# Kernel tuning notes

Hardware: AMD Instinct MI355X
Metric: run time of the kernel (lower is better)

## Reference

```python
import jax, jax.numpy as jnp
import numpy as np

N_NODES = 100000
INPUT_DIM = 512
OUTPUT_DIM = 128
N_EDGES = 300000


def setup_inputs() -> dict:
    key = jax.random.key(0)
    k1, k2, k3, k4, k5 = jax.random.split(key, 5)
    x = jax.random.normal(k1, (N_NODES, INPUT_DIM), dtype=jnp.float32)
    train_edges = jax.random.randint(k2, (N_EDGES, 2), 0, N_NODES, dtype=jnp.int64)
    train_false_edges = jax.random.randint(k3, (N_EDGES, 2), 0, N_NODES, dtype=jnp.int64)
    # learned params (xavier / kaiming init approximated with uniform fan-based scales)
    limit_w = float(np.sqrt(6.0 / (INPUT_DIM + OUTPUT_DIM)))
    weight = jax.random.uniform(k4, (INPUT_DIM, OUTPUT_DIM), dtype=jnp.float32,
                                minval=-limit_w, maxval=limit_w)
    limit_w3 = float(np.sqrt(6.0 / OUTPUT_DIM) / np.sqrt(2.0))
    weight_three = jax.random.uniform(k5, (OUTPUT_DIM, 1), dtype=jnp.float32,
                                      minval=-limit_w3, maxval=limit_w3)
    return {"x": x, "train_edges": train_edges, "train_false_edges": train_false_edges,
            "weight": weight, "weight_three": weight_three}


def _decode(z, edges, weight_three):
    # gather endpoints, elementwise multiply, matvec against weight_three
    prod = z[edges[:, 0]] * z[edges[:, 1]]  # [E, output_dim]
    return prod @ weight_three               # [E, 1]


def reference(x, train_edges, train_false_edges, weight, weight_three):
    z = x @ weight  # encode: [N, output_dim]
    z1 = _decode(z, train_edges, weight_three)
    z2 = _decode(z, train_false_edges, weight_three)
    return jax.nn.sigmoid(jnp.concatenate((z1, z2), axis=0))
```

## Files before the change

kernel.cpp:

```cpp
#include <hip/hip_runtime.h>
#include <math.h>

#define IN_DIM 512
#define OUT_DIM 128
#define BM 64
#define BK 64
#define NKT (IN_DIM / BK)

typedef __attribute__((ext_vector_type(8))) __bf16 bf16x8;
typedef __attribute__((ext_vector_type(2))) __bf16 bf16x2;
typedef __attribute__((ext_vector_type(4))) float f32x4;
typedef __attribute__((ext_vector_type(2))) float f32x2;

__device__ inline unsigned short f2bf(float f) {
    unsigned u = __float_as_uint(f);
    u += 0x7FFFu + ((u >> 16) & 1u);
    return (unsigned short)(u >> 16);
}

__device__ inline bf16x8 cvt8(const f32x4& lo, const f32x4& hi) {
    bf16x2 p0 = {(__bf16)lo.x, (__bf16)lo.y};
    bf16x2 p1 = {(__bf16)lo.z, (__bf16)lo.w};
    bf16x2 p2 = {(__bf16)hi.x, (__bf16)hi.y};
    bf16x2 p3 = {(__bf16)hi.z, (__bf16)hi.w};
    uint4 u = {__builtin_bit_cast(unsigned, p0), __builtin_bit_cast(unsigned, p1),
               __builtin_bit_cast(unsigned, p2), __builtin_bit_cast(unsigned, p3)};
    return __builtin_bit_cast(bf16x8, u);
}

__device__ inline void gload_lds16(const void* g, void* l) {
    __builtin_amdgcn_global_load_lds(
        (const __attribute__((address_space(1))) void*)g,
        (__attribute__((address_space(3))) void*)l, 16, 0, 0);
}

__global__ void wt2_kernel(const float* __restrict__ w, unsigned short* __restrict__ wt2) {
    int idx = blockIdx.x * 256 + threadIdx.x;
    int k = idx >> 7;
    int n = idx & 127;
    wt2[(((k >> 3) * 128) + n) * 8 + (k & 7)] = f2bf(w[idx]);
}

__global__ __launch_bounds__(256, 2) void gemm_mfma(const float* __restrict__ x,
                                                    const unsigned short* __restrict__ wt2,
                                                    unsigned short* __restrict__ zb,
                                                    int M) {
    __shared__ float sA[4][BM * BK / 4 * 4];
    char* const pAb = (char*)sA;

    const int tid  = threadIdx.x;
    const int lane = tid & 63;
    const int wid  = tid >> 6;
    const int wm   = wid >> 1;
    const int wn   = wid & 1;
    const int block_row = blockIdx.x * BM;

    const int fr  = lane & 15;
    const int fk4 = lane >> 4;

    f32x4 acc[2][4];
#pragma unroll
    for (int i = 0; i < 2; ++i)
#pragma unroll
        for (int j = 0; j < 4; ++j) acc[i][j] = (f32x4){0.f, 0.f, 0.f, 0.f};

    const int s_row = lane >> 4;
    const int s_cb  = (lane & 15) * 16;

    const int rowa0 = wm * 32 + fr;
    const int rowa1 = rowa0 + 16;
    const int swz7  = (fr & 7) << 5;

    const unsigned short* pb = wt2 + fk4 * 1024 + (wn * 64 + fr) * 8;

#define STAGE(T, B)                                                              \
    {                                                                            \
        _Pragma("unroll") for (int i = 0; i < 4; ++i) {                          \
            const int rr = (wid * 4 + i) * 4 + s_row;                            \
            int grow = block_row + rr;                                           \
            grow = (grow < M) ? grow : (M - 1);                                  \
            const char* src = (const char*)x + (size_t)grow * 2048 +             \
                              (T) * 256 + (s_cb ^ ((rr & 7) << 5));              \
            gload_lds16(src, pAb + (B) * 16384 + (wid * 4 + i) * 1024);          \
        }                                                                        \
    }

#define WAITB(N)                                                                 \
    {                                                                            \
        asm volatile("s_waitcnt vmcnt(" #N ")" ::: "memory");                    \
        __builtin_amdgcn_sched_barrier(0);                                       \
        __builtin_amdgcn_s_barrier();                                            \
        __builtin_amdgcn_sched_barrier(0);                                       \
    }

#define COMP(T, B)                                                               \
    {                                                                            \
        const char* pT = pAb + (B) * 16384;                                      \
        _Pragma("unroll") for (int ks = 0; ks < 2; ++ks) {                       \
            const int cb0 = ks * 128 + fk4 * 32;                                 \
            f32x4 lo0 = *(const f32x4*)(pT + rowa0 * 256 + (cb0 ^ swz7));        \
            f32x4 hi0 = *(const f32x4*)(pT + rowa0 * 256 + (cb0 ^ swz7) + 16);   \
            f32x4 lo1 = *(const f32x4*)(pT + rowa1 * 256 + (cb0 ^ swz7));        \
            f32x4 hi1 = *(const f32x4*)(pT + rowa1 * 256 + (cb0 ^ swz7) + 16);   \
            bf16x8 af0 = cvt8(lo0, hi0);                                         \
            bf16x8 af1 = cvt8(lo1, hi1);                                         \
            bf16x8 bv0 = *(const bf16x8*)(pb + (T) * 8192 + ks * 4096 + 0);      \
            bf16x8 bv1 = *(const bf16x8*)(pb + (T) * 8192 + ks * 4096 + 128);    \
            bf16x8 bv2 = *(const bf16x8*)(pb + (T) * 8192 + ks * 4096 + 256);    \
            bf16x8 bv3 = *(const bf16x8*)(pb + (T) * 8192 + ks * 4096 + 384);    \
            acc[0][0] = __builtin_amdgcn_mfma_f32_16x16x32_bf16(af0, bv0, acc[0][0], 0, 0, 0); \
            acc[0][1] = __builtin_amdgcn_mfma_f32_16x16x32_bf16(af0, bv1, acc[0][1], 0, 0, 0); \
            acc[0][2] = __builtin_amdgcn_mfma_f32_16x16x32_bf16(af0, bv2, acc[0][2], 0, 0, 0); \
            acc[0][3] = __builtin_amdgcn_mfma_f32_16x16x32_bf16(af0, bv3, acc[0][3], 0, 0, 0); \
            acc[1][0] = __builtin_amdgcn_mfma_f32_16x16x32_bf16(af1, bv0, acc[1][0], 0, 0, 0); \
            acc[1][1] = __builtin_amdgcn_mfma_f32_16x16x32_bf16(af1, bv1, acc[1][1], 0, 0, 0); \
            acc[1][2] = __builtin_amdgcn_mfma_f32_16x16x32_bf16(af1, bv2, acc[1][2], 0, 0, 0); \
            acc[1][3] = __builtin_amdgcn_mfma_f32_16x16x32_bf16(af1, bv3, acc[1][3], 0, 0, 0); \
        }                                                                        \
    }

    STAGE(0, 0);
    STAGE(1, 1);

    STAGE(2, 2); WAITB(8); COMP(0, 0);
    STAGE(3, 3); WAITB(8); COMP(1, 1);
    STAGE(4, 0); WAITB(8); COMP(2, 2);
    STAGE(5, 1); WAITB(8); COMP(3, 3);
    STAGE(6, 2); WAITB(8); COMP(4, 0);
    STAGE(7, 3); WAITB(8); COMP(5, 1);
                 WAITB(4); COMP(6, 2);
                 WAITB(0); COMP(7, 3);

#undef STAGE
#undef WAITB
#undef COMP

    const int crow0 = (lane >> 4) * 4;
    const int ccol  = lane & 15;
#pragma unroll
    for (int mf = 0; mf < 2; ++mf)
#pragma unroll
        for (int r = 0; r < 4; ++r) {
            const int grow = block_row + wm * 32 + mf * 16 + crow0 + r;
            if (grow < M) {
                unsigned short* zr = zb + (size_t)grow * OUT_DIM + wn * 64 + ccol;
#pragma unroll
                for (int nf = 0; nf < 4; ++nf)
                    zr[nf * 16] = f2bf(acc[mf][nf][r]);
            }
        }
}

__device__ inline float dotw3(const uint4& ua, const uint4& ub, const f32x2* w3v) {
    const unsigned pa[4] = {ua.x, ua.y, ua.z, ua.w};
    const unsigned pb[4] = {ub.x, ub.y, ub.z, ub.w};
    f32x2 vv = (f32x2){0.f, 0.f};
#pragma unroll
    for (int i = 0; i < 4; ++i) {
        f32x2 A = (f32x2){__uint_as_float(pa[i] << 16),
                          __uint_as_float(pa[i] & 0xFFFF0000u)};
        f32x2 B = (f32x2){__uint_as_float(pb[i] << 16),
                          __uint_as_float(pb[i] & 0xFFFF0000u)};
        vv += (A * B) * w3v[i];
    }
    return vv.x + vv.y;
}

__global__ __launch_bounds__(256) void decode_kernel(const unsigned short* __restrict__ zb,
                                                     const int* __restrict__ e1,
                                                     const int* __restrict__ e2,
                                                     const float* __restrict__ w3,
                                                     float* __restrict__ out,
                                                     int E1, int E2) {
    const int tid  = threadIdx.x;
    const int lane = tid & 63;
    const int sub  = lane & 15;
    const int sg   = lane >> 4;
    const int Etot = E1 + E2;
    const int nq   = (Etot + 3) >> 2;

    f32x2 w3v[4];
    {
        const float4 wlo = *(const float4*)(w3 + sub * 8);
        const float4 whi = *(const float4*)(w3 + sub * 8 + 4);
        w3v[0] = (f32x2){wlo.x, wlo.y};
        w3v[1] = (f32x2){wlo.z, wlo.w};
        w3v[2] = (f32x2){whi.x, whi.y};
        w3v[3] = (f32x2){whi.z, whi.w};
    }

    const int wave = blockIdx.x * 4 + (tid >> 6);
    const int S    = gridDim.x * 4;

    for (int q = wave; q < nq; q += 2 * S) {
        const int q2    = q + S;
        const bool has2 = (q2 < nq);

        const int e_a = q * 4 + sg;
        const int e_b = has2 ? (q2 * 4 + sg) : e_a;
        const int ca  = min(e_a, Etot - 1);
        const int cb  = min(e_b, Etot - 1);

        const int2 ia = (ca < E1) ? ((const int2*)e1)[ca] : ((const int2*)e2)[ca - E1];
        const int2 ib = (cb < E1) ? ((const int2*)e1)[cb] : ((const int2*)e2)[cb - E1];

        const uint4 a1 = *(const uint4*)(zb + (size_t)ia.x * OUT_DIM + sub * 8);
        const uint4 b1 = *(const uint4*)(zb + (size_t)ia.y * OUT_DIM + sub * 8);
        const uint4 a2 = *(const uint4*)(zb + (size_t)ib.x * OUT_DIM + sub * 8);
        const uint4 b2 = *(const uint4*)(zb + (size_t)ib.y * OUT_DIM + sub * 8);

        float v1 = dotw3(a1, b1, w3v);
        float v2 = dotw3(a2, b2, w3v);

        v1 += __shfl_xor(v1, 8);  v2 += __shfl_xor(v2, 8);
        v1 += __shfl_xor(v1, 4);  v2 += __shfl_xor(v2, 4);
        v1 += __shfl_xor(v1, 2);  v2 += __shfl_xor(v2, 2);
        v1 += __shfl_xor(v1, 1);  v2 += __shfl_xor(v2, 1);

        if (sub == 0) {
            if (e_a < Etot) out[e_a] = 1.f / (1.f + __expf(-v1));
            if (has2 && e_b < Etot) out[e_b] = 1.f / (1.f + __expf(-v2));
        }
    }
}

extern "C" void kernel_launch(void* const* d_in, const int* in_sizes, int n_in,
                              void* d_out, int out_size, void* d_ws, size_t ws_size,
                              hipStream_t stream) {
    const float* x  = (const float*)d_in[0];
    const int*   e1 = (const int*)d_in[1];
    const int*   e2 = (const int*)d_in[2];
    const float* w  = (const float*)d_in[3];
    const float* w3 = (const float*)d_in[4];

    float* out = (float*)d_out;

    const int M  = in_sizes[0] / IN_DIM;
    const int E1 = in_sizes[1] / 2;
    const int E2 = in_sizes[2] / 2;

    unsigned short* zbuf = (unsigned short*)d_ws;
    unsigned short* wt2  = zbuf + (size_t)M * OUT_DIM;

    wt2_kernel<<<(IN_DIM * OUT_DIM) / 256, 256, 0, stream>>>(w, wt2);
    gemm_mfma<<<(M + BM - 1) / BM, 256, 0, stream>>>(x, wt2, zbuf, M);
    decode_kernel<<<2048, 256, 0, stream>>>(zbuf, e1, e2, w3, out, E1, E2);
}
```

Baseline: 95.44 us.

## Double-buffer GEMM LDS, prefetch B into registers, swap MFMA operands for vector stores

Cuts the A-tile LDS ring from four stages to two, which halves shared memory so the kernel can target four blocks per SIMD instead of two. B fragments are now prefetched into registers one K-tile ahead rather than loaded inside the compute step. The MFMA operands are swapped so each lane holds four consecutive output columns, which lets the epilogue write packed 8-byte bf16 stores instead of scalar shorts. The cost is shallower prefetch depth, a full __syncthreads per K-tile, and more register pressure under the tighter launch bound.

```diff
diff --git a/kernel.cpp b/kernel.cpp
--- a/kernel.cpp
+++ b/kernel.cpp
@@ -16,6 +16,9 @@
     unsigned u = __float_as_uint(f);
     u += 0x7FFFu + ((u >> 16) & 1u);
     return (unsigned short)(u >> 16);
+}
+__device__ inline unsigned pack2f(float a, float b) {
+    return (unsigned)f2bf(a) | ((unsigned)f2bf(b) << 16);
 }
 
 __device__ inline bf16x8 cvt8(const f32x4& lo, const f32x4& hi) {
@@ -41,11 +44,11 @@
     wt2[(((k >> 3) * 128) + n) * 8 + (k & 7)] = f2bf(w[idx]);
 }
 
-__global__ __launch_bounds__(256, 2) void gemm_mfma(const float* __restrict__ x,
+__global__ __launch_bounds__(256, 4) void gemm_mfma(const float* __restrict__ x,
                                                     const unsigned short* __restrict__ wt2,
                                                     unsigned short* __restrict__ zb,
                                                     int M) {
-    __shared__ float sA[4][BM * BK / 4 * 4];
+    __shared__ float sA[2][BM * BK];
     char* const pAb = (char*)sA;
 
     const int tid  = threadIdx.x;
@@ -73,7 +76,23 @@
 
     const unsigned short* pb = wt2 + fk4 * 1024 + (wn * 64 + fr) * 8;
 
-#define STAGE(T, B)                                                              \
+    bf16x8 Ba0, Ba1, Ba2, Ba3;
+    bf16x8 Bb0, Bb1, Bb2, Bb3;
+    bf16x8 K10, K11, K12, K13;
+
+#define LOADB0(T, R0, R1, R2, R3)                         \
+    R0 = *(const bf16x8*)(pb + (T) * 8192 + 0);           \
+    R1 = *(const bf16x8*)(pb + (T) * 8192 + 128);         \
+    R2 = *(const bf16x8*)(pb + (T) * 8192 + 256);         \
+    R3 = *(const bf16x8*)(pb + (T) * 8192 + 384);
+
+#define LOADB1(T)                                         \
+    K10 = *(const bf16x8*)(pb + (T) * 8192 + 4096 + 0);   \
+    K11 = *(const bf16x8*)(pb + (T) * 8192 + 4096 + 128); \
+    K12 = *(const bf16x8*)(pb + (T) * 8192 + 4096 + 256); \
+    K13 = *(const bf16x8*)(pb + (T) * 8192 + 4096 + 384);
+
+#define STAGE(T, BUF)                                                            \
     {                                                                            \
         _Pragma("unroll") for (int i = 0; i < 4; ++i) {                          \
             const int rr = (wid * 4 + i) * 4 + s_row;                            \
@@ -81,74 +100,103 @@
             grow = (grow < M) ? grow : (M - 1);                                  \
             const char* src = (const char*)x + (size_t)grow * 2048 +             \
                               (T) * 256 + (s_cb ^ ((rr & 7) << 5));              \
-            gload_lds16(src, pAb + (B) * 16384 + (wid * 4 + i) * 1024);          \
+            gload_lds16(src, pAb + (BUF) * 16384 + (wid * 4 + i) * 1024);        \
         }                                                                        \
     }
 
-#define WAITB(N)                                                                 \
+#define COMP(BUF, B0, B1, B2, B3)                                                \
     {                                                                            \
-        asm volatile("s_waitcnt vmcnt(" #N ")" ::: "memory");                    \
-        __builtin_amdgcn_sched_barrier(0);                                       \
-        __builtin_amdgcn_s_barrier();                                            \
-        __builtin_amdgcn_sched_barrier(0);                                       \
-    }
-
-#define COMP(T, B)                                                               \
-    {                                                                            \
-        const char* pT = pAb + (B) * 16384;                                      \
-        _Pragma("unroll") for (int ks = 0; ks < 2; ++ks) {                       \
-            const int cb0 = ks * 128 + fk4 * 32;                                 \
-            f32x4 lo0 = *(const f32x4*)(pT + rowa0 * 256 + (cb0 ^ swz7));        \
-            f32x4 hi0 = *(const f32x4*)(pT + rowa0 * 256 + (cb0 ^ swz7) + 16);   \
-            f32x4 lo1 = *(const f32x4*)(pT + rowa1 * 256 + (cb0 ^ swz7));        \
-            f32x4 hi1 = *(const f32x4*)(pT + rowa1 * 256 + (cb0 ^ swz7) + 16);   \
+        const char* pT = pAb + (BUF) * 16384;                                    \
+                   \
+        {                                                                        \
+            const int cb = (fk4 * 32) ^ swz7;                                    \
+            f32x4 lo0 = *(const f32x4*)(pT + rowa0 * 256 + cb);                  \
+            f32x4 hi0 = *(const f32x4*)(pT + rowa0 * 256 + cb + 16);             \
+            f32x4 lo1 = *(const f32x4*)(pT + rowa1 * 256 + cb);                  \
+            f32x4 hi1 = *(const f32x4*)(pT + rowa1 * 256 + cb + 16);             \
             bf16x8 af0 = cvt8(lo0, hi0);                                         \
             bf16x8 af1 = cvt8(lo1, hi1);                                         \
-            bf16x8 bv0 = *(const bf16x8*)(pb + (T) * 8192 + ks * 4096 + 0);      \
-            bf16x8 bv1 = *(const bf16x8*)(pb + (T) * 8192 + ks * 4096 + 128);    \
-            bf16x8 bv2 = *(const bf16x8*)(pb + (T) * 8192 + ks * 4096 + 256);    \
-            bf16x8 bv3 = *(const bf16x8*)(pb + (T) * 8192 + ks * 4096 + 384);    \
-            acc[0][0] = __builtin_amdgcn_mfma_f32_16x16x32_bf16(af0, bv0, acc[0][0], 0, 0, 0); \
-            acc[0][1] = __builtin_amdgcn_mfma_f32_16x16x32_bf16(af0, bv1, acc[0][1], 0, 0, 0); \
-            acc[0][2] = __builtin_amdgcn_mfma_f32_16x16x32_bf16(af0, bv2, acc[0][2], 0, 0, 0); \
-            acc[0][3] = __builtin_amdgcn_mfma_f32_16x16x32_bf16(af0, bv3, acc[0][3], 0, 0, 0); \
-            acc[1][0] = __builtin_amdgcn_mfma_f32_16x16x32_bf16(af1, bv0, acc[1][0], 0, 0, 0); \
-            acc[1][1] = __builtin_amdgcn_mfma_f32_16x16x32_bf16(af1, bv1, acc[1][1], 0, 0, 0); \
-            acc[1][2] = __builtin_amdgcn_mfma_f32_16x16x32_bf16(af1, bv2, acc[1][2], 0, 0, 0); \
-            acc[1][3] = __builtin_amdgcn_mfma_f32_16x16x32_bf16(af1, bv3, acc[1][3], 0, 0, 0); \
+            acc[0][0] = __builtin_amdgcn_mfma_f32_16x16x32_bf16(B0, af0, acc[0][0], 0, 0, 0); \
+            acc[0][1] = __builtin_amdgcn_mfma_f32_16x16x32_bf16(B1, af0, acc[0][1], 0, 0, 0); \
+            acc[0][2] = __builtin_amdgcn_mfma_f32_16x16x32_bf16(B2, af0, acc[0][2], 0, 0, 0); \
+            acc[0][3] = __builtin_amdgcn_mfma_f32_16x16x32_bf16(B3, af0, acc[0][3], 0, 0, 0); \
+            acc[1][0] = __builtin_amdgcn_mfma_f32_16x16x32_bf16(B0, af1, acc[1][0], 0, 0, 0); \
+            acc[1][1] = __builtin_amdgcn_mfma_f32_16x16x32_bf16(B1, af1, acc[1][1], 0, 0, 0); \
+            acc[1][2] = __builtin_amdgcn_mfma_f32_16x16x32_bf16(B2, af1, acc[1][2], 0, 0, 0); \
+            acc[1][3] = __builtin_amdgcn_mfma_f32_16x16x32_bf16(B3, af1, acc[1][3], 0, 0, 0); \
         }                                                                        \
-    }
+                \
+        {                                                                        \
+            const int cb = (128 + fk4 * 32) ^ swz7;                              \
+            f32x4 lo0 = *(const f32x4*)(pT + rowa0 * 256 + cb);                  \
+            f32x4 hi0 = *(const f32x4*)(pT + rowa0 * 256 + cb + 16);             \
+            f32x4 lo1 = *(const f32x4*)(pT + rowa1 * 256 + cb);                  \
+            f32x4 hi1 = *(const f32x4*)(pT + rowa1 * 256 + cb + 16);             \
+            bf16x8 af0 = cvt8(lo0, hi0);                                         \
+            bf16x8 af1 = cvt8(lo1, hi1);                                         \
+            acc[0][0] = __builtin_amdgcn_mfma_f32_16x16x32_bf16(K10, af0, acc[0][0], 0, 0, 0); \
+            acc[0][1] = __builtin_amdgcn_mfma_f32_16x16x32_bf16(K11, af0, acc[0][1], 0, 0, 0); \
+            acc[0][2] = __builtin_amdgcn_mfma_f32_16x16x32_bf16(K12, af0, acc[0][2], 0, 0, 0); \
+            acc[0][3] = __builtin_amdgcn_mfma_f32_16x16x32_bf16(K13, af0, acc[0][3], 0, 0, 0); \
+            acc[1][0] = __builtin_amdgcn_mfma_f32_16x16x32_bf16(K10, af1, acc[1][0], 0, 0, 0); \
+            acc[1][1] = __builtin_amdgcn_mfma_f32_16x16x32_bf16(K11, af1, acc[1][1], 0, 0, 0); \
+            acc[1][2] = __builtin_amdgcn_mfma_f32_16x16x32_bf16(K12, af1, acc[1][2], 0, 0, 0); \
+            acc[1][3] = __builtin_amdgcn_mfma_f32_16x16x32_bf16(K13, af1, acc[1][3], 0, 0, 0); \
+        }                                                                        \
+    }
+
+#define SB __builtin_amdgcn_sched_barrier(0);
 
     STAGE(0, 0);
-    STAGE(1, 1);
-
-    STAGE(2, 2); WAITB(8); COMP(0, 0);
-    STAGE(3, 3); WAITB(8); COMP(1, 1);
-    STAGE(4, 0); WAITB(8); COMP(2, 2);
-    STAGE(5, 1); WAITB(8); COMP(3, 3);
-    STAGE(6, 2); WAITB(8); COMP(4, 0);
-    STAGE(7, 3); WAITB(8); COMP(5, 1);
-                 WAITB(4); COMP(6, 2);
-                 WAITB(0); COMP(7, 3);
-
+    LOADB0(0, Ba0, Ba1, Ba2, Ba3);
+    __syncthreads();
+
+    LOADB1(0); SB; LOADB0(1, Bb0, Bb1, Bb2, Bb3); STAGE(1, 1);
+    COMP(0, Ba0, Ba1, Ba2, Ba3); __syncthreads();
+
+    LOADB1(1); SB; LOADB0(2, Ba0, Ba1, Ba2, Ba3); STAGE(2, 0);
+    COMP(1, Bb0, Bb1, Bb2, Bb3); __syncthreads();
+
+    LOADB1(2); SB; LOADB0(3, Bb0, Bb1, Bb2, Bb3); STAGE(3, 1);
+    COMP(0, Ba0, Ba1, Ba2, Ba3); __syncthreads();
+
+    LOADB1(3); SB; LOADB0(4, Ba0, Ba1, Ba2, Ba3); STAGE(4, 0);
+    COMP(1, Bb0, Bb1, Bb2, Bb3); __syncthreads();
+
+    LOADB1(4); SB; LOADB0(5, Bb0, Bb1, Bb2, Bb3); STAGE(5, 1);
+    COMP(0, Ba0, Ba1, Ba2, Ba3); __syncthreads();
+
+    LOADB1(5); SB; LOADB0(6, Ba0, Ba1, Ba2, Ba3); STAGE(6, 0);
+    COMP(1, Bb0, Bb1, Bb2, Bb3); __syncthreads();
+
+    LOADB1(6); SB; LOADB0(7, Bb0, Bb1, Bb2, Bb3); STAGE(7, 1);
+    COMP(0, Ba0, Ba1, Ba2, Ba3); __syncthreads();
+
+    LOADB1(7); SB;
+    COMP(1, Bb0, Bb1, Bb2, Bb3);
+
+#undef LOADB0
+#undef LOADB1
 #undef STAGE
-#undef WAITB
 #undef COMP
-
-    const int crow0 = (lane >> 4) * 4;
-    const int ccol  = lane & 15;
-#pragma unroll
-    for (int mf = 0; mf < 2; ++mf)
-#pragma unroll
-        for (int r = 0; r < 4; ++r) {
-            const int grow = block_row + wm * 32 + mf * 16 + crow0 + r;
-            if (grow < M) {
-                unsigned short* zr = zb + (size_t)grow * OUT_DIM + wn * 64 + ccol;
-#pragma unroll
-                for (int nf = 0; nf < 4; ++nf)
-                    zr[nf * 16] = f2bf(acc[mf][nf][r]);
+#undef SB
+
+    const int cm  = lane & 15;
+    const int cn0 = (lane >> 4) * 4;
+#pragma unroll
+    for (int mf = 0; mf < 2; ++mf) {
+        const int grow = block_row + wm * 32 + mf * 16 + cm;
+        if (grow < M) {
+            unsigned short* zr = zb + (size_t)grow * OUT_DIM + wn * 64 + cn0;
+#pragma unroll
+            for (int nf = 0; nf < 4; ++nf) {
+                uint2 u;
+                u.x = pack2f(acc[mf][nf][0], acc[mf][nf][1]);
+                u.y = pack2f(acc[mf][nf][2], acc[mf][nf][3]);
+                *(uint2*)(zr + nf * 16) = u;
             }
         }
+    }
 }
 
 __device__ inline float dotw3(const uint4& ua, const uint4& ub, const f32x2* w3v) {
```

Measured after the change: 88.76 us. 7.0% less time.
